# Performance work log

Measured on AMD Instinct MI355X. Metric: run time of the kernel, lower is better.

## Reference

```python
import jax, jax.numpy as jnp
import numpy as np
import itertools

# config: dim=256, resolution=14, key_dim=32, heads=8, attention_ratio=4, act=gelu (exact)
B, DIM, RES = 128, 256, 14
H, KD, DV = 8, 32, 128          # heads, key_dim, int(attention_ratio*key_dim)
N = RES * RES                    # 196 tokens
DH = H * DV                      # dim_head = 1024
SCALE = KD ** -0.5


def _bias_idxs():
    points = list(itertools.product(range(RES), range(RES)))
    offsets, idxs = {}, []
    for p1 in points:
        for p2 in points:
            off = (abs(p1[0] - p2[0]), abs(p1[1] - p2[1]))
            if off not in offsets:
                offsets[off] = len(offsets)
            idxs.append(offsets[off])
    return np.asarray(idxs, np.int32).reshape(N, N), len(offsets)


def _cbn(x, w, b, s, t):
    # 1x1 conv (as channel GEMM) + inference BatchNorm folded to per-channel affine
    y = jnp.einsum('bchw,co->bohw', x, w) + b[None, :, None, None]
    return y * s[None, :, None, None] + t[None, :, None, None]


def setup_inputs() -> dict:
    key = jax.random.key(0)
    ks = jax.random.split(key, 32)
    n = lambda i, sh, sc=0.05: jax.random.normal(ks[i], sh, jnp.float32) * sc
    idxs, noff = _bias_idxs()
    return {
        'hidden_states': jax.random.normal(ks[0], (B, DIM, RES, RES), jnp.float32),
        'w_q': n(1, (DIM, H * KD)), 'b_q': n(2, (H * KD,)), 's_q': 1.0 + n(3, (H * KD,)), 't_q': n(4, (H * KD,)),
        'w_k': n(5, (DIM, H * KD)), 'b_k': n(6, (H * KD,)), 's_k': 1.0 + n(7, (H * KD,)), 't_k': n(8, (H * KD,)),
        'w_v': n(9, (DIM, DH)), 'b_v': n(10, (DH,)), 's_v': 1.0 + n(11, (DH,)), 't_v': n(12, (DH,)),
        'w_vl': n(13, (DH, 1, 3, 3)), 'b_vl': n(14, (DH,)), 's_vl': 1.0 + n(15, (DH,)), 't_vl': n(16, (DH,)),
        'w_th1': n(17, (H, H), 0.2), 'b_th1': n(18, (H,)),
        'w_th2': n(19, (H, H), 0.2), 'b_th2': n(20, (H,)),
        'w_p': n(21, (DH, DIM)), 'b_p': n(22, (DIM,)), 's_p': 1.0 + n(23, (DIM,)), 't_p': n(24, (DIM,)),
        'attention_biases': n(25, (H, noff), 0.2),
        'bias_idxs': jnp.asarray(idxs),
    }


def reference(hidden_states, w_q, b_q, s_q, t_q, w_k, b_k, s_k, t_k,
              w_v, b_v, s_v, t_v, w_vl, b_vl, s_vl, t_vl,
              w_th1, b_th1, w_th2, b_th2, w_p, b_p, s_p, t_p,
              attention_biases, bias_idxs):
    b = hidden_states.shape[0]
    q = _cbn(hidden_states, w_q, b_q, s_q, t_q).reshape(b, H, KD, N).transpose(0, 1, 3, 2)  # [B,H,N,kd]
    k = _cbn(hidden_states, w_k, b_k, s_k, t_k).reshape(b, H, KD, N)                        # [B,H,kd,N]
    v_img = _cbn(hidden_states, w_v, b_v, s_v, t_v)                                          # [B,DH,res,res]
    vl = jax.lax.conv_general_dilated(v_img, w_vl, (1, 1), ((1, 1), (1, 1)),
                                      feature_group_count=DH,
                                      dimension_numbers=('NCHW', 'OIHW', 'NCHW'))
    vl = (vl + b_vl[None, :, None, None]) * s_vl[None, :, None, None] + t_vl[None, :, None, None]
    v = v_img.reshape(b, H, DV, N).transpose(0, 1, 3, 2)                                     # [B,H,N,dv]

    ab = attention_biases[:, bias_idxs]                                                      # [H,N,N]
    attn = jnp.einsum('bhnk,bhkm->bhnm', q, k) * SCALE + ab[None]                            # [B,H,N,N]
    attn = jnp.einsum('gh,bhnm->bgnm', w_th1, attn) + b_th1[None, :, None, None]             # talking head 1
    attn = jax.nn.softmax(attn, axis=-1)
    attn = jnp.einsum('gh,bhnm->bgnm', w_th2, attn) + b_th2[None, :, None, None]             # talking head 2

    out = jnp.einsum('bhnm,bhmd->bhnd', attn, v)                                             # [B,H,N,dv]
    out = out.transpose(0, 1, 3, 2).reshape(b, DH, RES, RES) + vl
    out = jax.nn.gelu(out, approximate=False)                                                # torch GELU (exact)
    return _cbn(out, w_p, b_p, s_p, t_p)                                                     # [B,dim,res,res]
```

## Files before the change

### kernel.cpp

```cpp
#include <hip/hip_runtime.h>
#include <hip/hip_bf16.h>

typedef __hip_bfloat16 bf16;
typedef __attribute__((ext_vector_type(8))) short bf16x8;
typedef __attribute__((ext_vector_type(8))) unsigned short u16x8;
typedef __attribute__((ext_vector_type(4))) float f32x4;

#define NB 128
#define CIN 256
#define NPIX 196
#define RESW 14
#define NH 8
#define KD 32
#define DV 128
#define DHID 1024
#define QKSCALE 0.17677669529663687f
#define QT 16
#define NTILE 13
#define VSTRIDE 224
#define ZPAD 232
#define XSP 264
#define GROWS 208

__device__ __forceinline__ float bf2f(unsigned short u) {
  union { unsigned int i; float f; } x; x.i = ((unsigned int)u) << 16; return x.f;
}
__device__ __forceinline__ unsigned short f2bfs(float f) {
  union { float f; unsigned int i; } u; u.f = f;
  unsigned int r = u.i + 0x7fffu + ((u.i >> 16) & 1u);
  return (unsigned short)(r >> 16);
}
__device__ __forceinline__ float gelu_exact(float x) {
  return x * 0.5f * (1.f + erff(x * 0.70710678118654752f));
}

__global__ void k_fold(
    const float* wq, const float* bq, const float* sq, const float* tq,
    const float* wk, const float* bk, const float* sk, const float* tk,
    const float* wv, const float* bv, const float* sv, const float* tv,
    const float* wvl, const float* bvl_in, const float* svl, const float* tvl,
    const float* wp, const float* bp_in, const float* sp, const float* tp,
    const float* abias, const int* bidx, const float* w1, const float* b1,
    int noff,
    short* Wt, short* Wpt, float* bcat, float* bpf, float* Wvl, float* bvlf,
    float* AB1)
{
  int i = blockIdx.x * 256 + threadIdx.x;
  if (i < 393216) {
    int o = i >> 8, c = i & 255;
    float w, s;
    if (o < 256)      { w = wq[c * 256 + o];          s = sq[o]; }
    else if (o < 512) { w = wk[c * 256 + (o - 256)];  s = sk[o - 256]; }
    else              { w = wv[c * 1024 + (o - 512)]; s = sv[o - 512]; }
    Wt[i] = (short)f2bfs(w * s);
    return;
  }
  i -= 393216;
  if (i < 1536) {
    float b, s, t;
    if (i < 256)      { b = bq[i];        s = sq[i];        t = tq[i]; }
    else if (i < 512) { b = bk[i - 256];  s = sk[i - 256];  t = tk[i - 256]; }
    else              { b = bv[i - 512];  s = sv[i - 512];  t = tv[i - 512]; }
    bcat[i] = b * s + t;
    return;
  }
  i -= 1536;
  if (i < 262144) {
    int o = i >> 10, ch = i & 1023;
    Wpt[i] = (short)f2bfs(wp[ch * 256 + o] * sp[o]);
    return;
  }
  i -= 262144;
  if (i < 256) { bpf[i] = bp_in[i] * sp[i] + tp[i]; return; }
  i -= 256;
  if (i < 9216) { int ch = i / 9; Wvl[i] = wvl[i] * svl[ch]; return; }
  i -= 9216;
  if (i < 1024) { bvlf[i] = bvl_in[i] * svl[i] + tvl[i]; return; }
  i -= 1024;
  if (i < NPIX * NPIX) {
    int idx = bidx[i];
    float a[8];
#pragma unroll
    for (int h = 0; h < 8; ++h) a[h] = abias[h * noff + idx];
#pragma unroll
    for (int g = 0; g < 8; ++g) {
      float z = b1[g];
#pragma unroll
      for (int h = 0; h < 8; ++h) z += w1[g * 8 + h] * a[h];
      AB1[(size_t)g * NPIX * NPIX + i] = z;
    }
    return;
  }
}

__global__ __launch_bounds__(512) void k_qkv(
    const float* __restrict__ X, const short* __restrict__ Wt,
    const float* __restrict__ bcat, bf16* __restrict__ Yq,
    bf16* __restrict__ Yk, bf16* __restrict__ Yv)
{
  __shared__ short Xs[112 * XSP];
  int b = blockIdx.x >> 1, half = blockIdx.x & 1;
  int t = threadIdx.x;
  const float* Xb = X + (size_t)b * CIN * NPIX;

  for (int i = t; i < 256 * 28; i += 512) {
    int c = i / 28, j = i % 28;
    int ng = half * 112 + 4 * j;
    int lr = 4 * j;
    if (ng + 3 < NPIX) {
      float4 xv = *(const float4*)(Xb + c * NPIX + ng);
      Xs[(lr + 0) * XSP + c] = (short)f2bfs(xv.x);
      Xs[(lr + 1) * XSP + c] = (short)f2bfs(xv.y);
      Xs[(lr + 2) * XSP + c] = (short)f2bfs(xv.z);
      Xs[(lr + 3) * XSP + c] = (short)f2bfs(xv.w);
    } else {
#pragma unroll
      for (int e = 0; e < 4; ++e) {
        float v = (ng + e < NPIX) ? Xb[c * NPIX + ng + e] : 0.f;
        Xs[(lr + e) * XSP + c] = (short)f2bfs(v);
      }
    }
  }
  __syncthreads();

  int w = t >> 6, lane = t & 63, nl = lane & 15, grp = lane >> 4;
  int NTH = half ? 6 : 7;
  int ntb = half * 7;

  for (int mm = w; mm < 192; mm += 8) {
    if (mm < 64) {
      int ot = mm >> 1, sub = mm & 1;
      int lt0 = sub * 4;
      int ltN = sub ? (NTH - 4) : 4;
      const short* arow = Wt + (size_t)(ot * 16 + nl) * CIN;
      f32x4 acc[4];
#pragma unroll
      for (int s = 0; s < 4; ++s) acc[s] = (f32x4){0.f, 0.f, 0.f, 0.f};
#pragma unroll
      for (int kk = 0; kk < 8; ++kk) {
        bf16x8 af = *(const bf16x8*)(arow + kk * 32 + grp * 8);
#pragma unroll
        for (int s = 0; s < 4; ++s) {
          if (s < ltN) {
            bf16x8 bfr = *(const bf16x8*)(Xs + ((lt0 + s) * 16 + nl) * XSP + kk * 32 + grp * 8);
            acc[s] = __builtin_amdgcn_mfma_f32_16x16x32_bf16(af, bfr, acc[s], 0, 0, 0);
          }
        }
      }
      int o0 = ot * 16 + grp * 4;
      float4 bb = *(const float4*)(bcat + o0);
      unsigned short* dst = (unsigned short*)((o0 < 256) ? Yq : Yk);
      int ob = o0 & 255;
#pragma unroll
      for (int s = 0; s < 4; ++s) {
        if (s < ltN) {
          int n = (ntb + lt0 + s) * 16 + nl;
          if (n < NPIX) {
            ushort4 pk;
            pk.x = f2bfs(acc[s][0] + bb.x); pk.y = f2bfs(acc[s][1] + bb.y);
            pk.z = f2bfs(acc[s][2] + bb.z); pk.w = f2bfs(acc[s][3] + bb.w);
            *(ushort4*)(dst + ((size_t)b * NPIX + n) * CIN + ob) = pk;
          }
        }
      }
    } else {
      int mm2 = mm - 64;
      int cht = mm2 >> 1, sub = mm2 & 1;
      int lt0 = sub * 4;
      int ltN = sub ? (NTH - 4) : 4;
      int ch = cht * 16 + nl;
      const short* brow = Wt + (size_t)(512 + ch) * CIN;
      f32x4 acc[4];
#pragma unroll
      for (int s = 0; s < 4; ++s) acc[s] = (f32x4){0.f, 0.f, 0.f, 0.f};
#pragma unroll
      for (int kk = 0; kk < 8; ++kk) {
        bf16x8 bfr = *(const bf16x8*)(brow + kk * 32 + grp * 8);
#pragma unroll
        for (int s = 0; s < 4; ++s) {
          if (s < ltN) {
            bf16x8 af = *(const bf16x8*)(Xs + ((lt0 + s) * 16 + nl) * XSP + kk * 32 + grp * 8);
            acc[s] = __builtin_amdgcn_mfma_f32_16x16x32_bf16(af, bfr, acc[s], 0, 0, 0);
          }
        }
      }
      float bb = bcat[512 + ch];
#pragma unroll
      for (int s = 0; s < 4; ++s) {
        if (s < ltN) {
          int m0 = (ntb + lt0 + s) * 16 + grp * 4;
          if (m0 + 3 < NPIX) {
            ushort4 pk;
            pk.x = f2bfs(acc[s][0] + bb); pk.y = f2bfs(acc[s][1] + bb);
            pk.z = f2bfs(acc[s][2] + bb); pk.w = f2bfs(acc[s][3] + bb);
            *(ushort4*)((unsigned short*)Yv + ((size_t)b * DHID + ch) * VSTRIDE + m0) = pk;
          }
        }
      }
    }
  }
}

__global__ __launch_bounds__(512) void k_conv(
    const bf16* __restrict__ Yv, const float* __restrict__ Wvl,
    const float* __restrict__ bvlf, bf16* __restrict__ Gt)
{
  __shared__ short Vs[128 * ZPAD];
  int b = blockIdx.x >> 3, cg = blockIdx.x & 7;
  int t = threadIdx.x;
  const unsigned short* src = (const unsigned short*)Yv + ((size_t)b * DHID + cg * 128) * VSTRIDE;
  for (int i = t; i < 128 * 28; i += 512) {
    int ch = i / 28, j = i % 28;
    u16x8 v = *(const u16x8*)(src + ch * VSTRIDE + j * 8);
    *(u16x8*)(Vs + ch * ZPAD + j * 8) = v;
  }
  __syncthreads();

  int ch = t & 127, yg = t >> 7;
  int chg = cg * 128 + ch;
  float w9[9];
#pragma unroll
  for (int k = 0; k < 9; ++k) w9[k] = Wvl[chg * 9 + k];
  float bb = bvlf[chg];
  const short* row = Vs + ch * ZPAD;
  unsigned short* gbase = (unsigned short*)Gt + (size_t)b * GROWS * DHID + chg;

  int ylim = (yg == 3) ? 2 : 4;
  for (int yy = 0; yy < ylim; ++yy) {
    int y = yg * 4 + yy;
    float rw[3][14];
#pragma unroll
    for (int dy = 0; dy < 3; ++dy) {
      int ys = y + dy - 1;
      if (ys < 0 || ys >= RESW) {
#pragma unroll
        for (int x = 0; x < 14; ++x) rw[dy][x] = 0.f;
      } else {
#pragma unroll
        for (int x2 = 0; x2 < 7; ++x2) {
          unsigned int u = *(const unsigned int*)(row + ys * RESW + x2 * 2);
          rw[dy][x2 * 2]     = bf2f((unsigned short)(u & 0xffffu));
          rw[dy][x2 * 2 + 1] = bf2f((unsigned short)(u >> 16));
        }
      }
    }
#pragma unroll
    for (int x = 0; x < 14; ++x) {
      float a = bb;
#pragma unroll
      for (int dy = 0; dy < 3; ++dy)
#pragma unroll
        for (int dx = 0; dx < 3; ++dx) {
          int xx = x + dx - 1;
          if (xx >= 0 && xx < RESW) a += w9[dy * 3 + dx] * rw[dy][xx];
        }
      gbase[(size_t)(y * RESW + x) * DHID] = f2bfs(a);
    }
  }
}

__global__ __launch_bounds__(512) void k_attn(
    const bf16* __restrict__ Yq, const bf16* __restrict__ Yk,
    const bf16* __restrict__ Yv, const float* __restrict__ AB1,
    const float* __restrict__ w1, const float* __restrict__ w2,
    const float* __restrict__ b2, bf16* __restrict__ Gt)
{
  __shared__ short zb[NH][QT][ZPAD];
  __shared__ float red[8][NH][16];
  int id = blockIdx.x;
  int swz = (id & 7) * (NB * NTILE / 8) + (id >> 3);
  int b = swz / NTILE, tile = swz % NTILE;
  int n0 = tile * QT;
  int t = threadIdx.x;
  int w = t >> 6, lane = t & 63;
  int nl = lane & 15, grp = lane >> 4;
  int n = n0 + nl;
  int nA = (n < NPIX) ? n : (NPIX - 1);

  int t0 = w;
  int t1 = (w < 5) ? (w + 8) : ((w == 5) ? 13 : -1);

  const short* qrow = (const short*)Yq + ((size_t)b * NPIX + nA) * CIN;
  bf16x8 qf[8];
#pragma unroll
  for (int h = 0; h < 8; ++h) qf[h] = *(const bf16x8*)(qrow + h * 32 + grp * 8);

  const short* kbase = (const short*)Yk + (size_t)b * NPIX * CIN;
  const f32x4 NEG = (f32x4){-1e30f, -1e30f, -1e30f, -1e30f};
  f32x4 zm0[8], zm1[8];

#define DO_TILE(MT, ZM)                                                        \
  {                                                                            \
    int m0_ = (MT) * 16 + grp * 4;                                             \
    bool mv_ = (m0_ + 3) < NPIX;                                               \
    if ((MT) < 13) {                                                           \
      int mrow_ = (MT) * 16 + nl; if (mrow_ > NPIX - 1) mrow_ = NPIX - 1;      \
      const short* krow_ = kbase + (size_t)mrow_ * CIN + grp * 8;              \
      f32x4 zr_[8];                                                            \
      _Pragma("unroll")                                                        \
      for (int h = 0; h < 8; ++h) {                                            \
        bf16x8 kf_ = *(const bf16x8*)(krow_ + h * 32);                         \
        zr_[h] = __builtin_amdgcn_mfma_f32_16x16x32_bf16(                      \
            kf_, qf[h], (f32x4){0.f, 0.f, 0.f, 0.f}, 0, 0, 0);                 \
      }                                                                        \
      _Pragma("unroll")                                                        \
      for (int g = 0; g < 8; ++g) {                                            \
        if (mv_) {                                                             \
          f32x4 a_ = *(const f32x4*)(AB1 + ((size_t)g * NPIX + nA) * NPIX + m0_); \
          _Pragma("unroll")                                                    \
          for (int h = 0; h < 8; ++h) {                                        \
            float wgh_ = w1[g * 8 + h] * QKSCALE;                              \
            _Pragma("unroll")                                                  \
            for (int r = 0; r < 4; ++r) a_[r] += wgh_ * zr_[h][r];             \
          }                                                                    \
          ZM[g] = a_;                                                          \
        } else ZM[g] = NEG;                                                    \
      }                                                                        \
    } else {                                                                   \
      _Pragma("unroll")                                                        \
      for (int g = 0; g < 8; ++g) ZM[g] = NEG;                                 \
    }                                                                          \
  }

  DO_TILE(t0, zm0)
  if (t1 >= 0) { DO_TILE(t1, zm1) }
  else {
#pragma unroll
    for (int g = 0; g < 8; ++g) zm1[g] = NEG;
  }

  float mg[8];
#pragma unroll
  for (int g = 0; g < 8; ++g) {
    float m_ = fmaxf(fmaxf(zm0[g][0], zm0[g][1]), fmaxf(zm0[g][2], zm0[g][3]));
    m_ = fmaxf(m_, fmaxf(fmaxf(zm1[g][0], zm1[g][1]), fmaxf(zm1[g][2], zm1[g][3])));
    m_ = fmaxf(m_, __shfl_xor(m_, 16));
    m_ = fmaxf(m_, __shfl_xor(m_, 32));
    mg[g] = m_;
  }
  if (lane < 16) {
#pragma unroll
    for (int g = 0; g < 8; ++g) red[w][g][nl] = mg[g];
  }
  __syncthreads();
  float fmx[8];
#pragma unroll
  for (int g = 0; g < 8; ++g) {
    float m_ = red[0][g][nl];
#pragma unroll
    for (int ww = 1; ww < 8; ++ww) m_ = fmaxf(m_, red[ww][g][nl]);
    fmx[g] = m_;
  }
  float sg[8];
#pragma unroll
  for (int g = 0; g < 8; ++g) {
    float s_ = 0.f;
#pragma unroll
    for (int r = 0; r < 4; ++r) { zm0[g][r] = __expf(zm0[g][r] - fmx[g]); s_ += zm0[g][r]; }
#pragma unroll
    for (int r = 0; r < 4; ++r) { zm1[g][r] = __expf(zm1[g][r] - fmx[g]); s_ += zm1[g][r]; }
    s_ += __shfl_xor(s_, 16);
    s_ += __shfl_xor(s_, 32);
    sg[g] = s_;
  }
  __syncthreads();
  if (lane < 16) {
#pragma unroll
    for (int g = 0; g < 8; ++g) red[w][g][nl] = sg[g];
  }
  __syncthreads();
  float inv[8];
#pragma unroll
  for (int g = 0; g < 8; ++g) {
    float s_ = red[0][g][nl];
#pragma unroll
    for (int ww = 1; ww < 8; ++ww) s_ += red[ww][g][nl];
    inv[g] = 1.f / s_;
  }

#define WR_TILE(MT, ZM)                                                        \
  {                                                                            \
    int m0_ = (MT) * 16 + grp * 4;                                             \
    _Pragma("unroll")                                                          \
    for (int g = 0; g < 8; ++g) {                                              \
      ushort4 pk_;                                                             \
      pk_.x = f2bfs(ZM[g][0] * inv[g]); pk_.y = f2bfs(ZM[g][1] * inv[g]);      \
      pk_.z = f2bfs(ZM[g][2] * inv[g]); pk_.w = f2bfs(ZM[g][3] * inv[g]);      \
      *(ushort4*)&zb[g][nl][m0_] = pk_;                                        \
    }                                                                          \
  }
  WR_TILE(t0, zm0)
  if (t1 >= 0) WR_TILE(t1, zm1)

  unsigned short* gp = (unsigned short*)Gt + ((size_t)b * GROWS + nA) * DHID + w * DV;
  ushort4 cvv[8];
#pragma unroll
  for (int dt = 0; dt < 8; ++dt) cvv[dt] = *(const ushort4*)(gp + dt * 16 + grp * 4);
  __syncthreads();

  float w2r[8];
#pragma unroll
  for (int h = 0; h < 8; ++h) w2r[h] = w2[w * 8 + h];
  float b2j = b2[w];
  f32x4 accO[8];
#pragma unroll
  for (int dt = 0; dt < 8; ++dt) accO[dt] = (f32x4){0.f, 0.f, 0.f, 0.f};
  const short* vbase = (const short*)Yv + ((size_t)b * DHID + w * DV) * VSTRIDE;
#pragma unroll
  for (int ks = 0; ks < 7; ++ks) {
    int moff = ks * 32 + grp * 8;
    bf16x8 rd[8];
#pragma unroll
    for (int gg = 0; gg < 8; ++gg) rd[gg] = *(const bf16x8*)&zb[gg][nl][moff];
    bf16x8 Bf;
#pragma unroll
    for (int jj = 0; jj < 8; ++jj) {
      int m = moff + jj;
      float a = (m < NPIX) ? b2j : 0.f;
#pragma unroll
      for (int gg = 0; gg < 8; ++gg) a += w2r[gg] * bf2f((unsigned short)rd[gg][jj]);
      Bf[jj] = (short)f2bfs(a);
    }
#pragma unroll
    for (int dt = 0; dt < 8; ++dt) {
      bf16x8 Af = *(const bf16x8*)(vbase + (size_t)(dt * 16 + nl) * VSTRIDE + moff);
      accO[dt] = __builtin_amdgcn_mfma_f32_16x16x32_bf16(Af, Bf, accO[dt], 0, 0, 0);
    }
  }

  if (n < NPIX) {
#pragma unroll
    for (int dt = 0; dt < 8; ++dt) {
      ushort4 pk;
      float pre;
      pre = accO[dt][0] + bf2f(cvv[dt].x); pk.x = f2bfs(gelu_exact(pre));
      pre = accO[dt][1] + bf2f(cvv[dt].y); pk.y = f2bfs(gelu_exact(pre));
      pre = accO[dt][2] + bf2f(cvv[dt].z); pk.z = f2bfs(gelu_exact(pre));
      pre = accO[dt][3] + bf2f(cvv[dt].w); pk.w = f2bfs(gelu_exact(pre));
      *(ushort4*)(gp + dt * 16 + grp * 4) = pk;
    }
  }
}

__global__ __launch_bounds__(256) void k_proj(
    const bf16* __restrict__ Gt, const short* __restrict__ Wpt,
    const float* __restrict__ bpf, float* __restrict__ out)
{
  int b = blockIdx.x >> 1, half = blockIdx.x & 1;
  int t = threadIdx.x, w = t >> 6, lane = t & 63, nl = lane & 15, grp = lane >> 4;
  int ot0 = half * 8 + w;
  int ot1 = ot0 + 4;
  const short* a0 = Wpt + (size_t)(ot0 * 16 + nl) * DHID + grp * 8;
  const short* a1 = Wpt + (size_t)(ot1 * 16 + nl) * DHID + grp * 8;
  const short* bb = (const short*)Gt + (size_t)b * GROWS * DHID + (size_t)nl * DHID + grp * 8;
  f32x4 acc0[13], acc1[13];
#pragma unroll
  for (int i = 0; i < 13; ++i) {
    acc0[i] = (f32x4){0.f, 0.f, 0.f, 0.f};
    acc1[i] = (f32x4){0.f, 0.f, 0.f, 0.f};
  }
  for (int kk = 0; kk < 32; ++kk) {
    bf16x8 af0 = *(const bf16x8*)(a0 + kk * 32);
    bf16x8 af1 = *(const bf16x8*)(a1 + kk * 32);
#pragma unroll
    for (int nt = 0; nt < 13; ++nt) {
      bf16x8 bfr = *(const bf16x8*)(bb + (size_t)(nt * 16) * DHID + kk * 32);
      acc0[nt] = __builtin_amdgcn_mfma_f32_16x16x32_bf16(af0, bfr, acc0[nt], 0, 0, 0);
      acc1[nt] = __builtin_amdgcn_mfma_f32_16x16x32_bf16(af1, bfr, acc1[nt], 0, 0, 0);
    }
  }
  int o0 = ot0 * 16 + grp * 4;
  int o1 = ot1 * 16 + grp * 4;
  float4 b0 = *(const float4*)(bpf + o0);
  float4 b1v = *(const float4*)(bpf + o1);
  float b0a[4] = {b0.x, b0.y, b0.z, b0.w};
  float b1a[4] = {b1v.x, b1v.y, b1v.z, b1v.w};
#pragma unroll
  for (int nt = 0; nt < 13; ++nt) {
    int nn = nt * 16 + nl;
    if (nn < NPIX) {
#pragma unroll
      for (int r = 0; r < 4; ++r) {
        out[((size_t)b * CIN + o0 + r) * NPIX + nn] = acc0[nt][r] + b0a[r];
        out[((size_t)b * CIN + o1 + r) * NPIX + nn] = acc1[nt][r] + b1a[r];
      }
    }
  }
}

extern "C" void kernel_launch(void* const* d_in, const int* in_sizes, int n_in,
                              void* d_out, int out_size, void* d_ws, size_t ws_size,
                              hipStream_t stream) {
  const float* X    = (const float*)d_in[0];
  const float* wq   = (const float*)d_in[1];
  const float* bq   = (const float*)d_in[2];
  const float* sq   = (const float*)d_in[3];
  const float* tq   = (const float*)d_in[4];
  const float* wk   = (const float*)d_in[5];
  const float* bk   = (const float*)d_in[6];
  const float* sk   = (const float*)d_in[7];
  const float* tk   = (const float*)d_in[8];
  const float* wv   = (const float*)d_in[9];
  const float* bv   = (const float*)d_in[10];
  const float* sv   = (const float*)d_in[11];
  const float* tv   = (const float*)d_in[12];
  const float* wvl  = (const float*)d_in[13];
  const float* bvl  = (const float*)d_in[14];
  const float* svl  = (const float*)d_in[15];
  const float* tvl  = (const float*)d_in[16];
  const float* w1   = (const float*)d_in[17];
  const float* b1   = (const float*)d_in[18];
  const float* w2   = (const float*)d_in[19];
  const float* b2   = (const float*)d_in[20];
  const float* wp   = (const float*)d_in[21];
  const float* bpp  = (const float*)d_in[22];
  const float* sp   = (const float*)d_in[23];
  const float* tp   = (const float*)d_in[24];
  const float* ab   = (const float*)d_in[25];
  const int*   bidx = (const int*)d_in[26];
  int noff = in_sizes[25] / NH;

  short* Wt   = (short*)d_ws;
  short* Wpt  = Wt + 393216;
  float* bcat = (float*)(Wpt + 262144);
  float* bpf  = bcat + 1536;
  float* Wvl  = bpf + 256;
  float* bvlf = Wvl + 9216;
  float* AB1  = bvlf + 1024;
  short* Yq   = (short*)(AB1 + 307328);
  short* Yk   = Yq + (size_t)NB * NPIX * CIN;
  short* Yv   = Yk + (size_t)NB * NPIX * CIN;
  short* Gt   = Yv + (size_t)NB * DHID * VSTRIDE;

  k_fold<<<2758, 256, 0, stream>>>(wq, bq, sq, tq, wk, bk, sk, tk,
                                   wv, bv, sv, tv, wvl, bvl, svl, tvl,
                                   wp, bpp, sp, tp, ab, bidx, w1, b1, noff,
                                   Wt, Wpt, bcat, bpf, Wvl, bvlf, AB1);
  k_qkv<<<NB * 2, 512, 0, stream>>>(X, Wt, bcat, (bf16*)Yq, (bf16*)Yk, (bf16*)Yv);
  k_conv<<<NB * 8, 512, 0, stream>>>((const bf16*)Yv, Wvl, bvlf, (bf16*)Gt);
  k_attn<<<NB * NTILE, 512, 0, stream>>>((const bf16*)Yq, (const bf16*)Yk,
                                         (const bf16*)Yv, AB1, w1, w2, b2, (bf16*)Gt);
  k_proj<<<NB * 2, 256, 0, stream>>>((const bf16*)Gt, Wpt, bpf, (float*)d_out);
}
```

Before: 483.7 us.

## Split QKV into quarter-token blocks, restructure attention mixing, re-split projection

The QKV GEMM now launches four blocks per batch over token quarters instead of two halves, which halves the LDS footprint and doubles grid parallelism. In attention, the talking-head-1 mix is accumulated as each QK MFMA result is produced, without holding all eight head scores. Talking-head-2 mixing moves into the score write-out, so the PV loop reads pre-mixed probabilities directly, and launch bounds now ask for 4 blocks per CU. The projection kernel now uses 512 threads per block, with the two blocks per batch covering token halves rather than output-channel halves, which cuts accumulator registers per thread.

```diff
diff --git a/kernel.cpp b/kernel.cpp
--- a/kernel.cpp
+++ b/kernel.cpp
@@ -98,14 +98,19 @@
     const float* __restrict__ bcat, bf16* __restrict__ Yq,
     bf16* __restrict__ Yk, bf16* __restrict__ Yv)
 {
-  __shared__ short Xs[112 * XSP];
-  int b = blockIdx.x >> 1, half = blockIdx.x & 1;
+  __shared__ short Xs[64 * XSP];
+  int b = blockIdx.x >> 2, q = blockIdx.x & 3;
+  const int qs_[4] = {0, 4, 7, 10};
+  const int qc_[4] = {4, 3, 3, 3};
+  int qs = qs_[q], qc = qc_[q];
+  int rowbase = qs * 16, nrows = qc * 16;
   int t = threadIdx.x;
   const float* Xb = X + (size_t)b * CIN * NPIX;
 
-  for (int i = t; i < 256 * 28; i += 512) {
-    int c = i / 28, j = i % 28;
-    int ng = half * 112 + 4 * j;
+  int jn = nrows >> 2;
+  for (int i = t; i < 256 * jn; i += 512) {
+    int c = i / jn, j = i % jn;
+    int ng = rowbase + 4 * j;
     int lr = 4 * j;
     if (ng + 3 < NPIX) {
       float4 xv = *(const float4*)(Xb + c * NPIX + ng);
@@ -124,14 +129,10 @@
   __syncthreads();
 
   int w = t >> 6, lane = t & 63, nl = lane & 15, grp = lane >> 4;
-  int NTH = half ? 6 : 7;
-  int ntb = half * 7;
-
-  for (int mm = w; mm < 192; mm += 8) {
-    if (mm < 64) {
-      int ot = mm >> 1, sub = mm & 1;
-      int lt0 = sub * 4;
-      int ltN = sub ? (NTH - 4) : 4;
+
+  for (int mm = w; mm < 96; mm += 8) {
+    if (mm < 32) {
+      int ot = mm;
       const short* arow = Wt + (size_t)(ot * 16 + nl) * CIN;
       f32x4 acc[4];
 #pragma unroll
@@ -141,8 +142,8 @@
         bf16x8 af = *(const bf16x8*)(arow + kk * 32 + grp * 8);
 #pragma unroll
         for (int s = 0; s < 4; ++s) {
-          if (s < ltN) {
-            bf16x8 bfr = *(const bf16x8*)(Xs + ((lt0 + s) * 16 + nl) * XSP + kk * 32 + grp * 8);
+          if (s < qc) {
+            bf16x8 bfr = *(const bf16x8*)(Xs + (s * 16 + nl) * XSP + kk * 32 + grp * 8);
             acc[s] = __builtin_amdgcn_mfma_f32_16x16x32_bf16(af, bfr, acc[s], 0, 0, 0);
           }
         }
@@ -153,8 +154,8 @@
       int ob = o0 & 255;
 #pragma unroll
       for (int s = 0; s < 4; ++s) {
-        if (s < ltN) {
-          int n = (ntb + lt0 + s) * 16 + nl;
+        if (s < qc) {
+          int n = (qs + s) * 16 + nl;
           if (n < NPIX) {
             ushort4 pk;
             pk.x = f2bfs(acc[s][0] + bb.x); pk.y = f2bfs(acc[s][1] + bb.y);
@@ -164,10 +165,7 @@
         }
       }
     } else {
-      int mm2 = mm - 64;
-      int cht = mm2 >> 1, sub = mm2 & 1;
-      int lt0 = sub * 4;
-      int ltN = sub ? (NTH - 4) : 4;
+      int cht = mm - 32;
       int ch = cht * 16 + nl;
       const short* brow = Wt + (size_t)(512 + ch) * CIN;
       f32x4 acc[4];
@@ -178,8 +176,8 @@
         bf16x8 bfr = *(const bf16x8*)(brow + kk * 32 + grp * 8);
 #pragma unroll
         for (int s = 0; s < 4; ++s) {
-          if (s < ltN) {
-            bf16x8 af = *(const bf16x8*)(Xs + ((lt0 + s) * 16 + nl) * XSP + kk * 32 + grp * 8);
+          if (s < qc) {
+            bf16x8 af = *(const bf16x8*)(Xs + (s * 16 + nl) * XSP + kk * 32 + grp * 8);
             acc[s] = __builtin_amdgcn_mfma_f32_16x16x32_bf16(af, bfr, acc[s], 0, 0, 0);
           }
         }
@@ -187,8 +185,8 @@
       float bb = bcat[512 + ch];
 #pragma unroll
       for (int s = 0; s < 4; ++s) {
-        if (s < ltN) {
-          int m0 = (ntb + lt0 + s) * 16 + grp * 4;
+        if (s < qc) {
+          int m0 = (qs + s) * 16 + grp * 4;
           if (m0 + 3 < NPIX) {
             ushort4 pk;
             pk.x = f2bfs(acc[s][0] + bb); pk.y = f2bfs(acc[s][1] + bb);
@@ -259,7 +257,7 @@
   }
 }
 
-__global__ __launch_bounds__(512) void k_attn(
+__global__ __launch_bounds__(512, 4) void k_attn(
     const bf16* __restrict__ Yq, const bf16* __restrict__ Yk,
     const bf16* __restrict__ Yv, const float* __restrict__ AB1,
     const float* __restrict__ w1, const float* __restrict__ w2,
@@ -292,33 +290,27 @@
 #define DO_TILE(MT, ZM)                                                        \
   {                                                                            \
     int m0_ = (MT) * 16 + grp * 4;                                             \
-    bool mv_ = (m0_ + 3) < NPIX;                                               \
+    bool mv_ = ((MT) < 13) && (m0_ + 3 < NPIX);                                \
+    _Pragma("unroll")                                                          \
+    for (int g = 0; g < 8; ++g) {                                              \
+      ZM[g] = mv_ ? (*(const f32x4*)(AB1 + ((size_t)g * NPIX + nA) * NPIX + m0_)) \
+                  : NEG;                                                       \
+    }                                                                          \
     if ((MT) < 13) {                                                           \
       int mrow_ = (MT) * 16 + nl; if (mrow_ > NPIX - 1) mrow_ = NPIX - 1;      \
       const short* krow_ = kbase + (size_t)mrow_ * CIN + grp * 8;              \
-      f32x4 zr_[8];                                                            \
       _Pragma("unroll")                                                        \
       for (int h = 0; h < 8; ++h) {                                            \
         bf16x8 kf_ = *(const bf16x8*)(krow_ + h * 32);                         \
-        zr_[h] = __builtin_amdgcn_mfma_f32_16x16x32_bf16(                      \
+        f32x4 zr_ = __builtin_amdgcn_mfma_f32_16x16x32_bf16(                   \
             kf_, qf[h], (f32x4){0.f, 0.f, 0.f, 0.f}, 0, 0, 0);                 \
+        _Pragma("unroll")                                                      \
+        for (int g = 0; g < 8; ++g) {                                          \
+          float wgh_ = w1[g * 8 + h] * QKSCALE;                                \
+          _Pragma("unroll")                                                    \
+          for (int r = 0; r < 4; ++r) ZM[g][r] += wgh_ * zr_[r];               \
+        }                                                                      \
       }                                                                        \
-      _Pragma("unroll")                                                        \
-      for (int g = 0; g < 8; ++g) {                                            \
-        if (mv_) {                                                             \
-          f32x4 a_ = *(const f32x4*)(AB1 + ((size_t)g * NPIX + nA) * NPIX + m0_); \
-          _Pragma("unroll")                                                    \
-          for (int h = 0; h < 8; ++h) {                                        \
-            float wgh_ = w1[g * 8 + h] * QKSCALE;                              \
-            _Pragma("unroll")                                                  \
-            for (int r = 0; r < 4; ++r) a_[r] += wgh_ * zr_[h][r];             \
-          }                                                                    \
-          ZM[g] = a_;                                                          \
-        } else ZM[g] = NEG;                                                    \
-      }                                                                        \
-    } else {                                                                   \
-      _Pragma("unroll")                                                        \
-      for (int g = 0; g < 8; ++g) ZM[g] = NEG;                                 \
     }                                                                          \
   }
 
@@ -378,19 +370,40 @@
     inv[g] = 1.f / s_;
   }
 
-#define WR_TILE(MT, ZM)                                                        \
+#define MIX_WR(MT, ZM)                                                         \
   {                                                                            \
     int m0_ = (MT) * 16 + grp * 4;                                             \
+    bool v_ = (m0_ + 3 < NPIX);                                                \
+    float aj_[8][4];                                                           \
+    _Pragma("unroll")                                                          \
+    for (int j = 0; j < 8; ++j) {                                              \
+      float bj_ = b2[j];                                                       \
+      _Pragma("unroll")                                                        \
+      for (int r = 0; r < 4; ++r) aj_[j][r] = bj_;                             \
+    }                                                                          \
     _Pragma("unroll")                                                          \
     for (int g = 0; g < 8; ++g) {                                              \
+      float pr_[4];                                                            \
+      _Pragma("unroll")                                                        \
+      for (int r = 0; r < 4; ++r) pr_[r] = ZM[g][r] * inv[g];                  \
+      _Pragma("unroll")                                                        \
+      for (int j = 0; j < 8; ++j) {                                            \
+        float wj_ = w2[j * 8 + g];                                             \
+        _Pragma("unroll")                                                      \
+        for (int r = 0; r < 4; ++r) aj_[j][r] += wj_ * pr_[r];                 \
+      }                                                                        \
+    }                                                                          \
+    _Pragma("unroll")                                                          \
+    for (int j = 0; j < 8; ++j) {                                              \
       ushort4 pk_;                                                             \
-      pk_.x = f2bfs(ZM[g][0] * inv[g]); pk_.y = f2bfs(ZM[g][1] * inv[g]);      \
-      pk_.z = f2bfs(ZM[g][2] * inv[g]); pk_.w = f2bfs(ZM[g][3] * inv[g]);      \
-      *(ushort4*)&zb[g][nl][m0_] = pk_;                                        \
+      if (v_) { pk_.x = f2bfs(aj_[j][0]); pk_.y = f2bfs(aj_[j][1]);            \
+                pk_.z = f2bfs(aj_[j][2]); pk_.w = f2bfs(aj_[j][3]); }          \
+      else    { pk_.x = 0; pk_.y = 0; pk_.z = 0; pk_.w = 0; }                  \
+      *(ushort4*)&zb[j][nl][m0_] = pk_;                                        \
     }                                                                          \
   }
-  WR_TILE(t0, zm0)
-  if (t1 >= 0) WR_TILE(t1, zm1)
+  MIX_WR(t0, zm0)
+  if (t1 >= 0) { MIX_WR(t1, zm1) }
 
   unsigned short* gp = (unsigned short*)Gt + ((size_t)b * GROWS + nA) * DHID + w * DV;
   ushort4 cvv[8];
@@ -398,10 +411,6 @@
   for (int dt = 0; dt < 8; ++dt) cvv[dt] = *(const ushort4*)(gp + dt * 16 + grp * 4);
   __syncthreads();
 
-  float w2r[8];
-#pragma unroll
-  for (int h = 0; h < 8; ++h) w2r[h] = w2[w * 8 + h];
-  float b2j = b2[w];
   f32x4 accO[8];
 #pragma unroll
   for (int dt = 0; dt < 8; ++dt) accO[dt] = (f32x4){0.f, 0.f, 0.f, 0.f};
@@ -409,18 +418,7 @@
 #pragma unroll
   for (int ks = 0; ks < 7; ++ks) {
     int moff = ks * 32 + grp * 8;
-    bf16x8 rd[8];
-#pragma unroll
-    for (int gg = 0; gg < 8; ++gg) rd[gg] = *(const bf16x8*)&zb[gg][nl][moff];
-    bf16x8 Bf;
-#pragma unroll
-    for (int jj = 0; jj < 8; ++jj) {
-      int m = moff + jj;
-      float a = (m < NPIX) ? b2j : 0.f;
-#pragma unroll
-      for (int gg = 0; gg < 8; ++gg) a += w2r[gg] * bf2f((unsigned short)rd[gg][jj]);
-      Bf[jj] = (short)f2bfs(a);
-    }
+    bf16x8 Bf = *(const bf16x8*)&zb[w][nl][moff];
 #pragma unroll
     for (int dt = 0; dt < 8; ++dt) {
       bf16x8 Af = *(const bf16x8*)(vbase + (size_t)(dt * 16 + nl) * VSTRIDE + moff);
@@ -442,20 +440,22 @@
   }
 }
 
-__global__ __launch_bounds__(256) void k_proj(
+__global__ __launch_bounds__(512) void k_proj(
     const bf16* __restrict__ Gt, const short* __restrict__ Wpt,
     const float* __restrict__ bpf, float* __restrict__ out)
 {
-  int b = blockIdx.x >> 1, half = blockIdx.x & 1;
+  int b = blockIdx.x >> 1, nhalf = blockIdx.x & 1;
   int t = threadIdx.x, w = t >> 6, lane = t & 63, nl = lane & 15, grp = lane >> 4;
-  int ot0 = half * 8 + w;
-  int ot1 = ot0 + 4;
+  int ot0 = w, ot1 = w + 8;
+  int ntb = nhalf * 7;
+  int NTH = nhalf ? 6 : 7;
   const short* a0 = Wpt + (size_t)(ot0 * 16 + nl) * DHID + grp * 8;
   const short* a1 = Wpt + (size_t)(ot1 * 16 + nl) * DHID + grp * 8;
-  const short* bb = (const short*)Gt + (size_t)b * GROWS * DHID + (size_t)nl * DHID + grp * 8;
-  f32x4 acc0[13], acc1[13];
-#pragma unroll
-  for (int i = 0; i < 13; ++i) {
+  const short* bb = (const short*)Gt + (size_t)b * GROWS * DHID
+                  + (size_t)(ntb * 16 + nl) * DHID + grp * 8;
+  f32x4 acc0[7], acc1[7];
+#pragma unroll
+  for (int i = 0; i < 7; ++i) {
     acc0[i] = (f32x4){0.f, 0.f, 0.f, 0.f};
     acc1[i] = (f32x4){0.f, 0.f, 0.f, 0.f};
   }
@@ -463,10 +463,12 @@
     bf16x8 af0 = *(const bf16x8*)(a0 + kk * 32);
     bf16x8 af1 = *(const bf16x8*)(a1 + kk * 32);
 #pragma unroll
-    for (int nt = 0; nt < 13; ++nt) {
-      bf16x8 bfr = *(const bf16x8*)(bb + (size_t)(nt * 16) * DHID + kk * 32);
-      acc0[nt] = __builtin_amdgcn_mfma_f32_16x16x32_bf16(af0, bfr, acc0[nt], 0, 0, 0);
-      acc1[nt] = __builtin_amdgcn_mfma_f32_16x16x32_bf16(af1, bfr, acc1[nt], 0, 0, 0);
+    for (int nt = 0; nt < 7; ++nt) {
+      if (nt < NTH) {
+        bf16x8 bfr = *(const bf16x8*)(bb + (size_t)(nt * 16) * DHID + kk * 32);
+        acc0[nt] = __builtin_amdgcn_mfma_f32_16x16x32_bf16(af0, bfr, acc0[nt], 0, 0, 0);
+        acc1[nt] = __builtin_amdgcn_mfma_f32_16x16x32_bf16(af1, bfr, acc1[nt], 0, 0, 0);
+      }
     }
   }
   int o0 = ot0 * 16 + grp * 4;
@@ -476,13 +478,15 @@
   float b0a[4] = {b0.x, b0.y, b0.z, b0.w};
   float b1a[4] = {b1v.x, b1v.y, b1v.z, b1v.w};
 #pragma unroll
-  for (int nt = 0; nt < 13; ++nt) {
-    int nn = nt * 16 + nl;
-    if (nn < NPIX) {
-#pragma unroll
-      for (int r = 0; r < 4; ++r) {
-        out[((size_t)b * CIN + o0 + r) * NPIX + nn] = acc0[nt][r] + b0a[r];
-        out[((size_t)b * CIN + o1 + r) * NPIX + nn] = acc1[nt][r] + b1a[r];
+  for (int nt = 0; nt < 7; ++nt) {
+    if (nt < NTH) {
+      int nn = (ntb + nt) * 16 + nl;
+      if (nn < NPIX) {
+#pragma unroll
+        for (int r = 0; r < 4; ++r) {
+          out[((size_t)b * CIN + o0 + r) * NPIX + nn] = acc0[nt][r] + b0a[r];
+          out[((size_t)b * CIN + o1 + r) * NPIX + nn] = acc1[nt][r] + b1a[r];
+        }
       }
     }
   }
@@ -536,9 +540,9 @@
                                    wv, bv, sv, tv, wvl, bvl, svl, tvl,
                                    wp, bpp, sp, tp, ab, bidx, w1, b1, noff,
                                    Wt, Wpt, bcat, bpf, Wvl, bvlf, AB1);
-  k_qkv<<<NB * 2, 512, 0, stream>>>(X, Wt, bcat, (bf16*)Yq, (bf16*)Yk, (bf16*)Yv);
+  k_qkv<<<NB * 4, 512, 0, stream>>>(X, Wt, bcat, (bf16*)Yq, (bf16*)Yk, (bf16*)Yv);
   k_conv<<<NB * 8, 512, 0, stream>>>((const bf16*)Yv, Wvl, bvlf, (bf16*)Gt);
   k_attn<<<NB * NTILE, 512, 0, stream>>>((const bf16*)Yq, (const bf16*)Yk,
                                          (const bf16*)Yv, AB1, w1, w2, b2, (bf16*)Gt);
-  k_proj<<<NB * 2, 256, 0, stream>>>((const bf16*)Gt, Wpt, bpf, (float*)d_out);
-}
+  k_proj<<<NB * 2, 512, 0, stream>>>((const bf16*)Gt, Wpt, bpf, (float*)d_out);
+}
```

Result: no change. 489.5 us (+1.2%).
